# Performance work log

Hardware: AMD Instinct MI355X
Metric: run time of the kernel (lower is better)

Reference implementation:

```python
import jax, jax.numpy as jnp
import numpy as np

N, L, E = 2, 2048, 1024
H = 16
HD = E // H
FF = 4 * E
EPS = 1e-5


def _layer_norm(x, g, b):
    mu = jnp.mean(x, axis=-1, keepdims=True)
    var = jnp.mean((x - mu) ** 2, axis=-1, keepdims=True)
    return (x - mu) * jax.lax.rsqrt(var + EPS) * g + b


def setup_inputs() -> dict:
    key = jax.random.key(0)
    ks = jax.random.split(key, 9)
    s = 0.02
    return {
        "value": jax.random.normal(ks[0], (N, L, E), jnp.float32),
        "key": jax.random.normal(ks[1], (N, L, E), jnp.float32),
        "query": jax.random.normal(ks[2], (N, L, E), jnp.float32),
        "w_out": jax.random.normal(ks[3], (E, E), jnp.float32) * s,
        "b_out": jnp.zeros((E,), jnp.float32),
        "w1": jax.random.normal(ks[4], (E, FF), jnp.float32) * s,
        "b1": jnp.zeros((FF,), jnp.float32),
        "w2": jax.random.normal(ks[5], (FF, E), jnp.float32) * s,
        "b2": jnp.zeros((E,), jnp.float32),
        "g1": jnp.ones((E,), jnp.float32),
        "be1": jnp.zeros((E,), jnp.float32),
        "g2": jnp.ones((E,), jnp.float32),
        "be2": jnp.zeros((E,), jnp.float32),
    }


def reference(value, key, query, w_out, b_out, w1, b1, w2, b2, g1, be1, g2, be2):
    # NOTE: source module never applies its Q/K/V Linear layers (repo bug);
    # raw inputs are reshaped per-head and used directly.
    v = value.reshape(N, L, H, HD)
    k = key.reshape(N, L, H, HD)
    q = query.reshape(N, L, H, HD)
    # energy: [N, H, Lq, Lk]; scale is 1/sqrt(embed_size) per the source
    energy = jnp.einsum("nqhd,nkhd->nhqk", q, k)
    attn = jax.nn.softmax(energy / jnp.sqrt(jnp.float32(E)), axis=-1)
    out = jnp.einsum("nhql,nlhd->nqhd", attn, v).reshape(N, L, E)
    out = out @ w_out + b_out
    x = _layer_norm(out + query, g1, be1)
    ff = jax.nn.relu(x @ w1 + b1) @ w2 + b2
    return _layer_norm(ff + x, g2, be2)
```

## Files before the change

kernel.cpp:

```cpp
#include <hip/hip_runtime.h>
#include <hip/hip_bf16.h>

#define NB 2
#define LL 2048
#define EE 1024
#define HH 16
#define HDD 64
#define FFD 4096

typedef unsigned short ushort_t;
typedef __attribute__((ext_vector_type(8))) short short8;
typedef __attribute__((ext_vector_type(4))) float f32x4;

constexpr float LN_EPS = 1e-5f;
constexpr float QSCALE = 0.03125f * 1.44269504088896340736f;

__device__ inline ushort_t f2bf(float f) {
    union { __hip_bfloat16 b; ushort_t u; } v;
    v.b = __float2bfloat16(f);
    return v.u;
}
__device__ inline float bf2f(unsigned us) {
    union { unsigned u; float f; } v; v.u = us << 16; return v.f;
}
__device__ inline unsigned pk_hi16(float lo, float hi) {
    const unsigned sel = 0x07060302u;
    unsigned r;
    asm("v_perm_b32 %0, %1, %2, %3" : "=v"(r) : "v"(hi), "v"(lo), "s"(sel));
    return r;
}

__device__ inline void gload16(const void* g, void* lds) {
    __builtin_amdgcn_global_load_lds(
        (const __attribute__((address_space(1))) void*)g,
        (__attribute__((address_space(3))) void*)lds, 16, 0, 0);
}

__global__ __launch_bounds__(256) void k_cvt(
    const float* __restrict__ in, ushort_t* __restrict__ out)
{
    const int t = threadIdx.x;
    const int g = blockIdx.x * 32 + (t >> 3);
    const int n = g >> 15, h = (g >> 11) & 15, l2 = g & 2047;
    const int d0 = (t & 7) * 8;
    const float* src = in + ((size_t)(n * LL + l2) * HH + h) * HDD + d0;
    const float4 a = *(const float4*)src;
    const float4 b = *(const float4*)(src + 4);
    uint4 pk;
    pk.x = f2bf(a.x) | ((unsigned)f2bf(a.y) << 16);
    pk.y = f2bf(a.z) | ((unsigned)f2bf(a.w) << 16);
    pk.z = f2bf(b.x) | ((unsigned)f2bf(b.y) << 16);
    pk.w = f2bf(b.z) | ((unsigned)f2bf(b.w) << 16);
    *(uint4*)(out + (size_t)g * HDD + d0) = pk;
}

__global__ __launch_bounds__(256) void v_cvt_t(
    const float* __restrict__ in, ushort_t* __restrict__ out)
{
    __shared__ float T[64][68];
    const int lb = blockIdx.x, h = blockIdx.y, n = blockIdx.z;
    const int t = threadIdx.x;
    const int l0 = lb * 64;
    {
        const int r = t >> 2, c0 = (t & 3) * 16;
        const float* src = in + ((size_t)(n * LL + l0 + r) * HH + h) * HDD + c0;
#pragma unroll
        for (int i = 0; i < 4; ++i)
            *(float4*)&T[r][c0 + 4 * i] = *(const float4*)(src + 4 * i);
    }
    __syncthreads();
    {
        const int d = t >> 2, tq = t & 3;
        unsigned u[8];
#pragma unroll
        for (int k = 0; k < 8; ++k) {
            const int c0 = tq * 16 + 2 * k, c1 = c0 + 1;
            const int p0 = (((c0 >> 5) * 2 + ((c0 >> 2) & 1)) << 4) +
                           (((c0 >> 3) & 3) << 2) + (c0 & 3);
            const int p1 = (((c1 >> 5) * 2 + ((c1 >> 2) & 1)) << 4) +
                           (((c1 >> 3) & 3) << 2) + (c1 & 3);
            u[k] = f2bf(T[p0][d]) | ((unsigned)f2bf(T[p1][d]) << 16);
        }
        ushort_t* dst = out + ((size_t)(n * HH + h) * HDD + d) * LL + l0 + tq * 16;
        uint4 q0; q0.x = u[0]; q0.y = u[1]; q0.z = u[2]; q0.w = u[3];
        uint4 q1; q1.x = u[4]; q1.y = u[5]; q1.z = u[6]; q1.w = u[7];
        *(uint4*)(dst)     = q0;
        *(uint4*)(dst + 8) = q1;
    }
}

__global__ __launch_bounds__(256) void attn_mfma(
    const float* __restrict__ Qf,
    const ushort_t* __restrict__ Kh,
    const ushort_t* __restrict__ Vt,
    ushort_t* __restrict__ O)
{
    const int s = blockIdx.x;
    const int xcd = s & 7, seq = s >> 3;
    const int qb = seq & 31, tt = seq >> 5;
    const int h = ((tt & 1) << 3) | xcd;
    const int n = tt >> 1;

    const int t = threadIdx.x, w = t >> 6, l = t & 63;
    const int lr = l & 15, lg = l >> 4;

    __shared__ __align__(16) ushort_t Ks[2][64 * 64];
    __shared__ __align__(16) ushort_t Vs[2][64 * 64];

    const size_t hbase = ((size_t)n * HH + h) * LL * HDD;
    const size_t vbase = ((size_t)n * HH + h) * HDD * LL;
    const int q0 = qb * 64 + w * 16;

    short8 bq[2];
#pragma unroll
    for (int ks = 0; ks < 2; ++ks) {
        const float* qsrc = Qf + ((size_t)(n * LL + q0 + lr) * HH + h) * HDD
                               + ks * 32 + lg * 8;
        const float4 a = *(const float4*)qsrc;
        const float4 b = *(const float4*)(qsrc + 4);
        union { short8 s8; unsigned u[4]; } pk;
        pk.u[0] = f2bf(a.x * QSCALE) | ((unsigned)f2bf(a.y * QSCALE) << 16);
        pk.u[1] = f2bf(a.z * QSCALE) | ((unsigned)f2bf(a.w * QSCALE) << 16);
        pk.u[2] = f2bf(b.x * QSCALE) | ((unsigned)f2bf(b.y * QSCALE) << 16);
        pk.u[3] = f2bf(b.z * QSCALE) | ((unsigned)f2bf(b.w * QSCALE) << 16);
        bq[ks] = pk.s8;
    }

    union { short8 s8; ushort_t u[8]; } one_u;
#pragma unroll
    for (int i = 0; i < 8; ++i) one_u.u[i] = 0x3F80;
    const short8 ones = one_u.s8;

    f32x4 acco[4];
#pragma unroll
    for (int dn = 0; dn < 4; ++dn) {
        f32x4 z = {0.f, 0.f, 0.f, 0.f};
        acco[dn] = z;
    }
    f32x4 accp = {0.f, 0.f, 0.f, 0.f};

    const int id0 = w * 2;
#define STAGE(buf, kt)                                                         \
    {                                                                          \
        _Pragma("unroll")                                                      \
        for (int j = 0; j < 2; ++j) {                                          \
            const int id = (id0 + j) * 64 + l;                                 \
            const int r = id >> 3, c = id & 7;                                 \
            const int cs = c ^ (r & 7);                                        \
            gload16(Kh + hbase + (size_t)((kt) * 64 + r) * HDD + cs * 8,       \
                    (void*)(Ks[buf] + (id0 + j) * 512));                       \
            gload16(Vt + vbase + (size_t)r * LL + (kt) * 64 + cs * 8,          \
                    (void*)(Vs[buf] + (id0 + j) * 512));                       \
        }                                                                      \
    }

    constexpr int NT = LL / 64;
    STAGE(0, 0);
    STAGE(1, 1);
    asm volatile("s_waitcnt vmcnt(4)" ::: "memory");
    __builtin_amdgcn_sched_barrier(0);
    __builtin_amdgcn_s_barrier();

    const f32x4 z4 = {0.f, 0.f, 0.f, 0.f};

    for (int kt = 0; kt < NT; ++kt) {
        const int buf = kt & 1;

        f32x4 accs[4];
        __builtin_amdgcn_s_setprio(1);
        {
            short8 ak[4];
#pragma unroll
            for (int nk = 0; nk < 4; ++nk) {
                const int row = nk * 16 + lr;
                ak[nk] = *(const short8*)(
                    Ks[buf] + row * 64 + ((lg) ^ (row & 7)) * 8);
            }
#pragma unroll
            for (int nk = 0; nk < 4; ++nk)
                accs[nk] = __builtin_amdgcn_mfma_f32_16x16x32_bf16(
                    ak[nk], bq[0], z4, 0, 0, 0);
#pragma unroll
            for (int nk = 0; nk < 4; ++nk) {
                const int row = nk * 16 + lr;
                ak[nk] = *(const short8*)(
                    Ks[buf] + row * 64 + ((4 | lg) ^ (row & 7)) * 8);
            }
#pragma unroll
            for (int nk = 0; nk < 4; ++nk)
                accs[nk] = __builtin_amdgcn_mfma_f32_16x16x32_bf16(
                    ak[nk], bq[1], accs[nk], 0, 0, 0);
        }
        __builtin_amdgcn_s_setprio(0);

        float p[4][4];
#pragma unroll
        for (int nk = 0; nk < 4; ++nk)
#pragma unroll
            for (int r = 0; r < 4; ++r)
                p[nk][r] = __builtin_amdgcn_exp2f(accs[nk][r]);
        short8 pa[2];
#pragma unroll
        for (int ks = 0; ks < 2; ++ks) {
            union { short8 s8; unsigned u[4]; } pk;
            pk.u[0] = pk_hi16(p[2*ks][0],   p[2*ks][1]);
            pk.u[1] = pk_hi16(p[2*ks][2],   p[2*ks][3]);
            pk.u[2] = pk_hi16(p[2*ks+1][0], p[2*ks+1][1]);
            pk.u[3] = pk_hi16(p[2*ks+1][2], p[2*ks+1][3]);
            pa[ks] = pk.s8;
        }

        __builtin_amdgcn_s_setprio(1);
#pragma unroll
        for (int ks = 0; ks < 2; ++ks) {
            short8 bv[4];
#pragma unroll
            for (int dn = 0; dn < 4; ++dn) {
                const int row = dn * 16 + lr;
                bv[dn] = *(const short8*)(
                    Vs[buf] + row * 64 + (((ks << 2) | lg) ^ (row & 7)) * 8);
            }
            accp = __builtin_amdgcn_mfma_f32_16x16x32_bf16(pa[ks], ones, accp,
                                                           0, 0, 0);
#pragma unroll
            for (int dn = 0; dn < 4; ++dn)
                acco[dn] = __builtin_amdgcn_mfma_f32_16x16x32_bf16(
                    pa[ks], bv[dn], acco[dn], 0, 0, 0);
        }
        __builtin_amdgcn_s_setprio(0);

        __builtin_amdgcn_s_barrier();
        STAGE(buf, kt + 2);
        asm volatile("s_waitcnt vmcnt(4)" ::: "memory");
        __builtin_amdgcn_sched_barrier(0);
        __builtin_amdgcn_s_barrier();
    }

#pragma unroll
    for (int r = 0; r < 4; ++r) {
        const float invl = 1.f / accp[r];
        const int qq = q0 + lg * 4 + r;
        ushort_t* dst = O + (size_t)(n * LL + qq) * EE + h * HDD + lr;
#pragma unroll
        for (int dn = 0; dn < 4; ++dn)
            dst[dn * 16] = f2bf(acco[dn][r] * invl);
    }
#undef STAGE
}

__global__ __launch_bounds__(256) void tcvt(
    const float* __restrict__ in, ushort_t* __restrict__ out, int K, int N)
{
    __shared__ float T[32][36];
    const int n0 = blockIdx.x * 32, k0 = blockIdx.y * 32;
    const int r = threadIdx.x >> 3, c4 = (threadIdx.x & 7) * 4;
    const float4 v = *(const float4*)(in + (size_t)(k0 + r) * N + n0 + c4);
    T[r][c4] = v.x; T[r][c4 + 1] = v.y; T[r][c4 + 2] = v.z; T[r][c4 + 3] = v.w;
    __syncthreads();
    const unsigned a = f2bf(T[c4][r])     | ((unsigned)f2bf(T[c4 + 1][r]) << 16);
    const unsigned b = f2bf(T[c4 + 2][r]) | ((unsigned)f2bf(T[c4 + 3][r]) << 16);
    uint2 pk; pk.x = a; pk.y = b;
    *(uint2*)(out + (size_t)(n0 + r) * K + k0 + c4) = pk;
}

__global__ __launch_bounds__(512, 2) void gemm8p(
    const ushort_t* __restrict__ A, const ushort_t* __restrict__ Bt,
    const float* __restrict__ bias, ushort_t* __restrict__ C,
    int M, int N, int K)
{
    __shared__ __align__(16) ushort_t L[2][4][256 * 32];

    const int tid = threadIdx.x;
    const int w = tid >> 6, l = tid & 63;
    const int fr = l & 15, lg = l >> 4;
    const int wr = w >> 2, wc = w & 3;

    const int gx = gridDim.x;
    const int nwg = gx * gridDim.y;
    const int bid = blockIdx.y * gx + blockIdx.x;
    int tile = bid;
    if ((nwg & 7) == 0) tile = (bid & 7) * (nwg >> 3) + (bid >> 3);
    const int bx = tile % gx, by = tile / gx;
    const int brow = by * 256, bcol = bx * 256;

    const int NT = K >> 6;
    const int UMAX = NT << 2;

#define STAGE8(u)                                                              \
    if ((u) < UMAX) {                                                          \
        const int tt = (u) >> 2, slot = (u) & 3;                               \
        const int op = slot & 1, kh = slot >> 1;                               \
        const ushort_t* sp = op ? Bt : A;                                      \
        const int rb = op ? bcol : brow;                                       \
        ushort_t* db = (ushort_t*)L[tt & 1][slot];                             \
        _Pragma("unroll")                                                      \
        for (int j = 0; j < 2; ++j) {                                          \
            const int id = j * 512 + tid;                                      \
            const int row = id >> 2, c = id & 3;                               \
            const int cs = c ^ ((row >> 1) & 3);                               \
            gload16(sp + (size_t)(rb + row) * K + tt * 64 + kh * 32 + cs * 8,  \
                    (void*)(db + id * 8));                                     \
        }                                                                      \
    }

    f32x4 acc[8][4];
#pragma unroll
    for (int i = 0; i < 8; ++i)
#pragma unroll
        for (int g = 0; g < 4; ++g) { f32x4 zz = {0.f,0.f,0.f,0.f}; acc[i][g] = zz; }

#pragma unroll
    for (int u = 0; u < 6; ++u) STAGE8(u);
    asm volatile("s_waitcnt vmcnt(4)" ::: "memory");
    __builtin_amdgcn_sched_barrier(0);
    __builtin_amdgcn_s_barrier();

    const int iters = NT >> 1;
    for (int it = 0; it < iters; ++it) {
#pragma unroll
        for (int p = 0; p < 8; ++p) {
            STAGE8(it * 8 + p + 6);
            const int d  = p >> 2;
            const int mh = p & 1, kh = (p >> 1) & 1;
            short8 af[4], bfr[4];
#pragma unroll
            for (int f = 0; f < 4; ++f) {
                const int row = wr * 128 + (mh * 4 + f) * 16 + fr;
                const int ch = lg ^ ((row >> 1) & 3);
                af[f] = *(const short8*)(&L[d][kh * 2][row * 32 + ch * 8]);
            }
#pragma unroll
            for (int g = 0; g < 4; ++g) {
                const int row = wc * 64 + g * 16 + fr;
                const int ch = lg ^ ((row >> 1) & 3);
                bfr[g] = *(const short8*)(&L[d][kh * 2 + 1][row * 32 + ch * 8]);
            }
            __builtin_amdgcn_s_barrier();
            __builtin_amdgcn_s_setprio(1);
#pragma unroll
            for (int f = 0; f < 4; ++f)
#pragma unroll
                for (int g = 0; g < 4; ++g)
                    acc[mh * 4 + f][g] = __builtin_amdgcn_mfma_f32_16x16x32_bf16(
                        af[f], bfr[g], acc[mh * 4 + f][g], 0, 0, 0);
            __builtin_amdgcn_s_setprio(0);
            if (p == 3 || p == 7) {
                asm volatile("s_waitcnt vmcnt(4)" ::: "memory");
                __builtin_amdgcn_sched_barrier(0);
            }
            __builtin_amdgcn_s_barrier();
        }
    }

#pragma unroll
    for (int mi = 0; mi < 8; ++mi) {
#pragma unroll
        for (int g = 0; g < 4; ++g) {
            const int col = bcol + wc * 64 + g * 16 + fr;
            const float bv = bias[col];
#pragma unroll
            for (int r = 0; r < 4; ++r) {
                const int row = brow + wr * 128 + mi * 16 + lg * 4 + r;
                const float v = fmaxf(acc[mi][g][r] + bv, 0.f);
                C[(size_t)row * N + col] = f2bf(v);
            }
        }
    }
#undef STAGE8
}

#define SOFF(slot) ((slot) == 0 ? 0 : (slot) == 1 ? 8192 : (slot) == 2 ? 12288 : 20480)

template <int KSPLIT>
__global__ __launch_bounds__(512, 2) void gemm8p_n128(
    const ushort_t* __restrict__ A, const ushort_t* __restrict__ Bt,
    ushort_t* __restrict__ C, int M, int N, int K)
{
    __shared__ __align__(16) ushort_t L[2][24576];

    const int tid = threadIdx.x;
    const int w = tid >> 6, l = tid & 63;
    const int fr = l & 15, lg = l >> 4;
    const int wr = w >> 2, wc = w & 3;

    const int z = blockIdx.z;
    const int Keff = K / KSPLIT;
    const int kb = z * Keff;

    const int gx = gridDim.x;
    const int nwg = gx * gridDim.y;
    const int bid = blockIdx.y * gx + blockIdx.x;
    int tile = bid;
    if ((nwg & 7) == 0) tile = (bid & 7) * (nwg >> 3) + (bid >> 3);
    const int bx = tile % gx, by = tile / gx;
    const int brow = by * 256, bcol = bx * 128;

    const int NT = Keff >> 6;
    const int UMAX = NT << 2;

#define STG(u)                                                                 \
    if ((u) < UMAX) {                                                          \
        const int tt = (u) >> 2, slot = (u) & 3;                               \
        const int op = slot & 1, kh = slot >> 1;                               \
        const ushort_t* sp = op ? Bt : A;                                      \
        const int rb = op ? bcol : brow;                                       \
        ushort_t* db = (ushort_t*)L[tt & 1] + SOFF(slot);                      \
        const int nld = op ? 1 : 2;                                            \
        _Pragma("unroll")                                                      \
        for (int j = 0; j < nld; ++j) {                                        \
            const int id = j * 512 + tid;                                      \
            const int row = id >> 2, c = id & 3;                               \
            const int cs = c ^ ((row >> 1) & 3);                               \
            gload16(sp + (size_t)(rb + row) * K + kb + tt * 64 + kh * 32 + cs * 8, \
                    (void*)(db + id * 8));                                     \
        }                                                                      \
    }

    f32x4 acc[8][2];
#pragma unroll
    for (int i = 0; i < 8; ++i)
#pragma unroll
        for (int g = 0; g < 2; ++g) { f32x4 zz = {0.f,0.f,0.f,0.f}; acc[i][g] = zz; }

#pragma unroll
    for (int u = 0; u < 6; ++u) STG(u);
    asm volatile("s_waitcnt vmcnt(3)" ::: "memory");
    __builtin_amdgcn_sched_barrier(0);
    __builtin_amdgcn_s_barrier();

    const int iters = NT >> 1;
    for (int it = 0; it < iters; ++it) {
#pragma unroll
        for (int p = 0; p < 8; ++p) {
            STG(it * 8 + p + 6);
            const int d  = p >> 2;
            const int mh = p & 1, kh = (p >> 1) & 1;
            short8 af[4], bfr[2];
#pragma unroll
            for (int f = 0; f < 4; ++f) {
                const int row = wr * 128 + (mh * 4 + f) * 16 + fr;
                const int ch = lg ^ ((row >> 1) & 3);
                af[f] = *(const short8*)(&L[d][SOFF(kh * 2) + row * 32 + ch * 8]);
            }
#pragma unroll
            for (int g = 0; g < 2; ++g) {
                const int row = wc * 32 + g * 16 + fr;
                const int ch = lg ^ ((row >> 1) & 3);
                bfr[g] = *(const short8*)(&L[d][SOFF(kh * 2 + 1) + row * 32 + ch * 8]);
            }
            __builtin_amdgcn_s_barrier();
            __builtin_amdgcn_s_setprio(1);
#pragma unroll
            for (int f = 0; f < 4; ++f)
#pragma unroll
                for (int g = 0; g < 2; ++g)
                    acc[mh * 4 + f][g] = __builtin_amdgcn_mfma_f32_16x16x32_bf16(
                        af[f], bfr[g], acc[mh * 4 + f][g], 0, 0, 0);
            __builtin_amdgcn_s_setprio(0);
            if (p == 3 || p == 7) {
                asm volatile("s_waitcnt vmcnt(3)" ::: "memory");
                __builtin_amdgcn_sched_barrier(0);
            }
            __builtin_amdgcn_s_barrier();
        }
    }

    ushort_t* Cb = C + (size_t)z * M * N;
#pragma unroll
    for (int mi = 0; mi < 8; ++mi) {
#pragma unroll
        for (int g = 0; g < 2; ++g) {
            const int col = bcol + wc * 32 + g * 16 + fr;
#pragma unroll
            for (int r = 0; r < 4; ++r) {
                const int row = brow + wr * 128 + mi * 16 + lg * 4 + r;
                Cb[(size_t)row * N + col] = f2bf(acc[mi][g][r]);
            }
        }
    }
#undef STG
}

__global__ __launch_bounds__(256) void ln_mid(
    const ushort_t* __restrict__ y0, const ushort_t* __restrict__ y1,
    const float* __restrict__ qres, const float* __restrict__ b0,
    const float* __restrict__ g, const float* __restrict__ b,
    ushort_t* __restrict__ out)
{
    const int row = blockIdx.x;
    const int t = threadIdx.x;
    const size_t off = (size_t)row * EE;
    const uint2 a = ((const uint2*)(y0 + off))[t];
    const uint2 c = ((const uint2*)(y1 + off))[t];
    const float4 qq = ((const float4*)(qres + off))[t];
    const float4 b04 = ((const float4*)b0)[t];
    float x[4];
    x[0] = bf2f(a.x & 0xffff) + bf2f(c.x & 0xffff) + qq.x + b04.x;
    x[1] = bf2f(a.x >> 16)    + bf2f(c.x >> 16)    + qq.y + b04.y;
    x[2] = bf2f(a.y & 0xffff) + bf2f(c.y & 0xffff) + qq.z + b04.z;
    x[3] = bf2f(a.y >> 16)    + bf2f(c.y >> 16)    + qq.w + b04.w;

    float s = 0.f, ss = 0.f;
#pragma unroll
    for (int i = 0; i < 4; ++i) { s += x[i]; ss += x[i] * x[i]; }
#pragma unroll
    for (int o = 1; o < 64; o <<= 1) {
        s  += __shfl_xor(s, o, 64);
        ss += __shfl_xor(ss, o, 64);
    }
    __shared__ float sm[8];
    const int wid = t >> 6;
    if ((t & 63) == 0) { sm[wid * 2] = s; sm[wid * 2 + 1] = ss; }
    __syncthreads();
    const float stot  = sm[0] + sm[2] + sm[4] + sm[6];
    const float sstot = sm[1] + sm[3] + sm[5] + sm[7];
    const float mu  = stot * (1.f / EE);
    const float inv = rsqrtf(sstot * (1.f / EE) - mu * mu + LN_EPS);

    const float4 gg = ((const float4*)g)[t];
    const float4 bb = ((const float4*)b)[t];
    uint2 pk;
    pk.x = f2bf((x[0] - mu) * inv * gg.x + bb.x) |
           ((unsigned)f2bf((x[1] - mu) * inv * gg.y + bb.y) << 16);
    pk.y = f2bf((x[2] - mu) * inv * gg.z + bb.z) |
           ((unsigned)f2bf((x[3] - mu) * inv * gg.w + bb.w) << 16);
    ((uint2*)(out + off))[t] = pk;
}

__global__ __launch_bounds__(256) void ln_out(
    const ushort_t* __restrict__ y0, const ushort_t* __restrict__ y1,
    const ushort_t* __restrict__ xb, const float* __restrict__ b2,
    const float* __restrict__ g, const float* __restrict__ be,
    float* __restrict__ out)
{
    const int row = blockIdx.x;
    const int t = threadIdx.x;
    const size_t off = (size_t)row * EE;
    const uint2 a = ((const uint2*)(y0 + off))[t];
    const uint2 b = ((const uint2*)(y1 + off))[t];
    const uint2 c = ((const uint2*)(xb + off))[t];
    const float4 bb2 = ((const float4*)b2)[t];
    float x[4];
    x[0] = bf2f(a.x & 0xffff) + bf2f(b.x & 0xffff) + bf2f(c.x & 0xffff) + bb2.x;
    x[1] = bf2f(a.x >> 16)    + bf2f(b.x >> 16)    + bf2f(c.x >> 16)    + bb2.y;
    x[2] = bf2f(a.y & 0xffff) + bf2f(b.y & 0xffff) + bf2f(c.y & 0xffff) + bb2.z;
    x[3] = bf2f(a.y >> 16)    + bf2f(b.y >> 16)    + bf2f(c.y >> 16)    + bb2.w;

    float s = 0.f, ss = 0.f;
#pragma unroll
    for (int i = 0; i < 4; ++i) { s += x[i]; ss += x[i] * x[i]; }
#pragma unroll
    for (int o = 1; o < 64; o <<= 1) {
        s  += __shfl_xor(s, o, 64);
        ss += __shfl_xor(ss, o, 64);
    }
    __shared__ float sm[8];
    const int wid = t >> 6;
    if ((t & 63) == 0) { sm[wid * 2] = s; sm[wid * 2 + 1] = ss; }
    __syncthreads();
    const float stot  = sm[0] + sm[2] + sm[4] + sm[6];
    const float sstot = sm[1] + sm[3] + sm[5] + sm[7];
    const float mu  = stot * (1.f / EE);
    const float inv = rsqrtf(sstot * (1.f / EE) - mu * mu + LN_EPS);

    const float4 gg = ((const float4*)g)[t];
    const float4 bb = ((const float4*)be)[t];
    float4 o;
    o.x = (x[0] - mu) * inv * gg.x + bb.x;
    o.y = (x[1] - mu) * inv * gg.y + bb.y;
    o.z = (x[2] - mu) * inv * gg.z + bb.z;
    o.w = (x[3] - mu) * inv * gg.w + bb.w;
    ((float4*)(out + off))[t] = o;
}

extern "C" void kernel_launch(void* const* d_in, const int* in_sizes, int n_in,
                              void* d_out, int out_size, void* d_ws, size_t ws_size,
                              hipStream_t stream) {
    (void)in_sizes; (void)n_in; (void)out_size; (void)ws_size;
    const float* value = (const float*)d_in[0];
    const float* key   = (const float*)d_in[1];
    const float* query = (const float*)d_in[2];
    const float* w_out = (const float*)d_in[3];
    const float* b_out = (const float*)d_in[4];
    const float* w1    = (const float*)d_in[5];
    const float* b1    = (const float*)d_in[6];
    const float* w2    = (const float*)d_in[7];
    const float* b2    = (const float*)d_in[8];
    const float* g1    = (const float*)d_in[9];
    const float* be1   = (const float*)d_in[10];
    const float* g2    = (const float*)d_in[11];
    const float* be2   = (const float*)d_in[12];
    float* out = (float*)d_out;

    const int M = NB * LL;
    char* base = (char*)d_ws;
    ushort_t* attn_bf = (ushort_t*)(base);
    ushort_t* x_bf    = (ushort_t*)(base + (8ull  << 20));
    char*     hregion = base + (16ull << 20);
    ushort_t* h_bf    = (ushort_t*)hregion;
    ushort_t* Kh      = (ushort_t*)(hregion);
    ushort_t* Vt      = (ushort_t*)(hregion + (8ull  << 20));
    ushort_t* y01     = (ushort_t*)(base + (48ull << 20));
    ushort_t* w0T     = (ushort_t*)(base + (64ull << 20));
    ushort_t* w1T     = (ushort_t*)(base + (66ull << 20));
    ushort_t* w2T     = (ushort_t*)(base + (74ull << 20));

    tcvt<<<dim3(EE / 32, EE / 32), 256, 0, stream>>>(w_out, w0T, EE, EE);
    tcvt<<<dim3(FFD / 32, EE / 32), 256, 0, stream>>>(w1, w1T, EE, FFD);
    tcvt<<<dim3(EE / 32, FFD / 32), 256, 0, stream>>>(w2, w2T, FFD, EE);

    k_cvt<<<NB * HH * LL / 32, 256, 0, stream>>>(key, Kh);
    v_cvt_t<<<dim3(LL / 64, HH, NB), 256, 0, stream>>>(value, Vt);

    attn_mfma<<<dim3(NB * HH * LL / 64), 256, 0, stream>>>(query, Kh, Vt,
                                                           attn_bf);

    gemm8p_n128<2><<<dim3(EE / 128, M / 256, 2), 512, 0, stream>>>(
        attn_bf, w0T, y01, M, EE, EE);
    ln_mid<<<M, 256, 0, stream>>>(y01, y01 + (size_t)M * EE, query, b_out,
                                  g1, be1, x_bf);

    gemm8p<<<dim3(FFD / 256, M / 256), 512, 0, stream>>>(x_bf, w1T, b1, h_bf,
                                                         M, FFD, EE);
    gemm8p_n128<2><<<dim3(EE / 128, M / 256, 2), 512, 0, stream>>>(
        h_bf, w2T, y01, M, EE, FFD);
    ln_out<<<M, 256, 0, stream>>>(y01, y01 + (size_t)M * EE, x_bf, b2, g2, be2,
                                  out);
}
```

Baseline: 189.7 us.

## Process two query sub-tiles per warp in attention to reuse K/V fragments

Each warp in the attention kernel now handles 32 query rows (two 16-row sub-tiles) instead of 16, so each block covers 128 queries and the grid is halved. K and V fragments loaded from shared memory are reused across both sub-tiles, which halves LDS reads and global K/V staging per unit of work. In exchange, register pressure roughly doubles for the accumulators and only 512 blocks are launched, which lowers occupancy and parallelism across CUs.

```diff
diff --git a/kernel.cpp b/kernel.cpp
--- a/kernel.cpp
+++ b/kernel.cpp
@@ -97,7 +97,7 @@
 {
     const int s = blockIdx.x;
     const int xcd = s & 7, seq = s >> 3;
-    const int qb = seq & 31, tt = seq >> 5;
+    const int qb = seq & 15, tt = seq >> 4;
     const int h = ((tt & 1) << 3) | xcd;
     const int n = tt >> 1;
 
@@ -109,35 +109,42 @@
 
     const size_t hbase = ((size_t)n * HH + h) * LL * HDD;
     const size_t vbase = ((size_t)n * HH + h) * HDD * LL;
-    const int q0 = qb * 64 + w * 16;
-
-    short8 bq[2];
-#pragma unroll
-    for (int ks = 0; ks < 2; ++ks) {
-        const float* qsrc = Qf + ((size_t)(n * LL + q0 + lr) * HH + h) * HDD
-                               + ks * 32 + lg * 8;
-        const float4 a = *(const float4*)qsrc;
-        const float4 b = *(const float4*)(qsrc + 4);
-        union { short8 s8; unsigned u[4]; } pk;
-        pk.u[0] = f2bf(a.x * QSCALE) | ((unsigned)f2bf(a.y * QSCALE) << 16);
-        pk.u[1] = f2bf(a.z * QSCALE) | ((unsigned)f2bf(a.w * QSCALE) << 16);
-        pk.u[2] = f2bf(b.x * QSCALE) | ((unsigned)f2bf(b.y * QSCALE) << 16);
-        pk.u[3] = f2bf(b.z * QSCALE) | ((unsigned)f2bf(b.w * QSCALE) << 16);
-        bq[ks] = pk.s8;
-    }
+    const int q0 = qb * 128 + w * 32;
+
+    short8 bq[2][2];
+#pragma unroll
+    for (int mi = 0; mi < 2; ++mi)
+#pragma unroll
+        for (int ks = 0; ks < 2; ++ks) {
+            const float* qsrc = Qf +
+                ((size_t)(n * LL + q0 + mi * 16 + lr) * HH + h) * HDD
+                + ks * 32 + lg * 8;
+            const float4 a = *(const float4*)qsrc;
+            const float4 b = *(const float4*)(qsrc + 4);
+            union { short8 s8; unsigned u[4]; } pk;
+            pk.u[0] = f2bf(a.x * QSCALE) | ((unsigned)f2bf(a.y * QSCALE) << 16);
+            pk.u[1] = f2bf(a.z * QSCALE) | ((unsigned)f2bf(a.w * QSCALE) << 16);
+            pk.u[2] = f2bf(b.x * QSCALE) | ((unsigned)f2bf(b.y * QSCALE) << 16);
+            pk.u[3] = f2bf(b.z * QSCALE) | ((unsigned)f2bf(b.w * QSCALE) << 16);
+            bq[mi][ks] = pk.s8;
+        }
 
     union { short8 s8; ushort_t u[8]; } one_u;
 #pragma unroll
     for (int i = 0; i < 8; ++i) one_u.u[i] = 0x3F80;
     const short8 ones = one_u.s8;
 
-    f32x4 acco[4];
-#pragma unroll
-    for (int dn = 0; dn < 4; ++dn) {
-        f32x4 z = {0.f, 0.f, 0.f, 0.f};
-        acco[dn] = z;
-    }
-    f32x4 accp = {0.f, 0.f, 0.f, 0.f};
+    f32x4 acco[2][4];
+#pragma unroll
+    for (int mi = 0; mi < 2; ++mi)
+#pragma unroll
+        for (int dn = 0; dn < 4; ++dn) {
+            f32x4 z = {0.f, 0.f, 0.f, 0.f};
+            acco[mi][dn] = z;
+        }
+    f32x4 accp[2];
+    accp[0] = (f32x4){0.f, 0.f, 0.f, 0.f};
+    accp[1] = (f32x4){0.f, 0.f, 0.f, 0.f};
 
     const int id0 = w * 2;
 #define STAGE(buf, kt)                                                         \
@@ -166,7 +173,7 @@
     for (int kt = 0; kt < NT; ++kt) {
         const int buf = kt & 1;
 
-        f32x4 accs[4];
+        f32x4 accs[2][4];
         __builtin_amdgcn_s_setprio(1);
         {
             short8 ak[4];
@@ -177,9 +184,12 @@
                     Ks[buf] + row * 64 + ((lg) ^ (row & 7)) * 8);
             }
 #pragma unroll
-            for (int nk = 0; nk < 4; ++nk)
-                accs[nk] = __builtin_amdgcn_mfma_f32_16x16x32_bf16(
-                    ak[nk], bq[0], z4, 0, 0, 0);
+            for (int nk = 0; nk < 4; ++nk) {
+                accs[0][nk] = __builtin_amdgcn_mfma_f32_16x16x32_bf16(
+                    ak[nk], bq[0][0], z4, 0, 0, 0);
+                accs[1][nk] = __builtin_amdgcn_mfma_f32_16x16x32_bf16(
+                    ak[nk], bq[1][0], z4, 0, 0, 0);
+            }
 #pragma unroll
             for (int nk = 0; nk < 4; ++nk) {
                 const int row = nk * 16 + lr;
@@ -187,27 +197,33 @@
                     Ks[buf] + row * 64 + ((4 | lg) ^ (row & 7)) * 8);
             }
 #pragma unroll
+            for (int nk = 0; nk < 4; ++nk) {
+                accs[0][nk] = __builtin_amdgcn_mfma_f32_16x16x32_bf16(
+                    ak[nk], bq[0][1], accs[0][nk], 0, 0, 0);
+                accs[1][nk] = __builtin_amdgcn_mfma_f32_16x16x32_bf16(
+                    ak[nk], bq[1][1], accs[1][nk], 0, 0, 0);
+            }
+        }
+        __builtin_amdgcn_s_setprio(0);
+
+        short8 pa[2][2];
+#pragma unroll
+        for (int mi = 0; mi < 2; ++mi) {
+            float p[4][4];
+#pragma unroll
             for (int nk = 0; nk < 4; ++nk)
-                accs[nk] = __builtin_amdgcn_mfma_f32_16x16x32_bf16(
-                    ak[nk], bq[1], accs[nk], 0, 0, 0);
-        }
-        __builtin_amdgcn_s_setprio(0);
-
-        float p[4][4];
-#pragma unroll
-        for (int nk = 0; nk < 4; ++nk)
-#pragma unroll
-            for (int r = 0; r < 4; ++r)
-                p[nk][r] = __builtin_amdgcn_exp2f(accs[nk][r]);
-        short8 pa[2];
-#pragma unroll
-        for (int ks = 0; ks < 2; ++ks) {
-            union { short8 s8; unsigned u[4]; } pk;
-            pk.u[0] = pk_hi16(p[2*ks][0],   p[2*ks][1]);
-            pk.u[1] = pk_hi16(p[2*ks][2],   p[2*ks][3]);
-            pk.u[2] = pk_hi16(p[2*ks+1][0], p[2*ks+1][1]);
-            pk.u[3] = pk_hi16(p[2*ks+1][2], p[2*ks+1][3]);
-            pa[ks] = pk.s8;
+#pragma unroll
+                for (int r = 0; r < 4; ++r)
+                    p[nk][r] = __builtin_amdgcn_exp2f(accs[mi][nk][r]);
+#pragma unroll
+            for (int ks = 0; ks < 2; ++ks) {
+                union { short8 s8; unsigned u[4]; } pk;
+                pk.u[0] = pk_hi16(p[2*ks][0],   p[2*ks][1]);
+                pk.u[1] = pk_hi16(p[2*ks][2],   p[2*ks][3]);
+                pk.u[2] = pk_hi16(p[2*ks+1][0], p[2*ks+1][1]);
+                pk.u[3] = pk_hi16(p[2*ks+1][2], p[2*ks+1][3]);
+                pa[mi][ks] = pk.s8;
+            }
         }
 
         __builtin_amdgcn_s_setprio(1);
@@ -220,12 +236,17 @@
                 bv[dn] = *(const short8*)(
                     Vs[buf] + row * 64 + (((ks << 2) | lg) ^ (row & 7)) * 8);
             }
-            accp = __builtin_amdgcn_mfma_f32_16x16x32_bf16(pa[ks], ones, accp,
-                                                           0, 0, 0);
-#pragma unroll
-            for (int dn = 0; dn < 4; ++dn)
-                acco[dn] = __builtin_amdgcn_mfma_f32_16x16x32_bf16(
-                    pa[ks], bv[dn], acco[dn], 0, 0, 0);
+            accp[0] = __builtin_amdgcn_mfma_f32_16x16x32_bf16(
+                pa[0][ks], ones, accp[0], 0, 0, 0);
+            accp[1] = __builtin_amdgcn_mfma_f32_16x16x32_bf16(
+                pa[1][ks], ones, accp[1], 0, 0, 0);
+#pragma unroll
+            for (int dn = 0; dn < 4; ++dn) {
+                acco[0][dn] = __builtin_amdgcn_mfma_f32_16x16x32_bf16(
+                    pa[0][ks], bv[dn], acco[0][dn], 0, 0, 0);
+                acco[1][dn] = __builtin_amdgcn_mfma_f32_16x16x32_bf16(
+                    pa[1][ks], bv[dn], acco[1][dn], 0, 0, 0);
+            }
         }
         __builtin_amdgcn_s_setprio(0);
 
@@ -237,13 +258,16 @@
     }
 
 #pragma unroll
-    for (int r = 0; r < 4; ++r) {
-        const float invl = 1.f / accp[r];
-        const int qq = q0 + lg * 4 + r;
-        ushort_t* dst = O + (size_t)(n * LL + qq) * EE + h * HDD + lr;
-#pragma unroll
-        for (int dn = 0; dn < 4; ++dn)
-            dst[dn * 16] = f2bf(acco[dn][r] * invl);
+    for (int mi = 0; mi < 2; ++mi) {
+#pragma unroll
+        for (int r = 0; r < 4; ++r) {
+            const float invl = 1.f / accp[mi][r];
+            const int qq = q0 + mi * 16 + lg * 4 + r;
+            ushort_t* dst = O + (size_t)(n * LL + qq) * EE + h * HDD + lr;
+#pragma unroll
+            for (int dn = 0; dn < 4; ++dn)
+                dst[dn * 16] = f2bf(acco[mi][dn][r] * invl);
+        }
     }
 #undef STAGE
 }
@@ -612,8 +636,8 @@
     k_cvt<<<NB * HH * LL / 32, 256, 0, stream>>>(key, Kh);
     v_cvt_t<<<dim3(LL / 64, HH, NB), 256, 0, stream>>>(value, Vt);
 
-    attn_mfma<<<dim3(NB * HH * LL / 64), 256, 0, stream>>>(query, Kh, Vt,
-                                                           attn_bf);
+    attn_mfma<<<dim3(NB * HH * LL / 128), 256, 0, stream>>>(query, Kh, Vt,
+                                                            attn_bf);
 
     gemm8p_n128<2><<<dim3(EE / 128, M / 256, 2), 512, 0, stream>>>(
         attn_bf, w0T, y01, M, EE, EE);
```

Result: faster. 186.0 us (-2.0%).

## Software-pipeline QK^T one tile ahead of PV with triple-buffered K

Applied to the files above, without the earlier changes.

Restructures the attention main loop so the QK^T MFMAs for the next key tile are issued before the exp/PV work of the current tile. K gets a third LDS buffer and V keeps two, and the loop is manually unrolled by two to ping-pong the score accumulators. The goal is to overlap the matrix-core work with the exp2 and pack ALU work and hide LDS latency. The cost is more LDS, more live registers, and a more complex K/V prefetch schedule. The prefetch also runs past the end of the sequence, as the original loop already did.

```diff
diff --git a/kernel.cpp b/kernel.cpp
--- a/kernel.cpp
+++ b/kernel.cpp
@@ -104,8 +104,8 @@
     const int t = threadIdx.x, w = t >> 6, l = t & 63;
     const int lr = l & 15, lg = l >> 4;
 
-    __shared__ __align__(16) ushort_t Ks[2][64 * 64];
-    __shared__ __align__(16) ushort_t Vs[2][64 * 64];
+    __shared__ __align__(16) ushort_t Kl[3][64 * 64];
+    __shared__ __align__(16) ushort_t Vl[2][64 * 64];
 
     const size_t hbase = ((size_t)n * HH + h) * LL * HDD;
     const size_t vbase = ((size_t)n * HH + h) * HDD * LL;
@@ -140,7 +140,7 @@
     f32x4 accp = {0.f, 0.f, 0.f, 0.f};
 
     const int id0 = w * 2;
-#define STAGE(buf, kt)                                                         \
+#define STAGEK(buf, kt)                                                        \
     {                                                                          \
         _Pragma("unroll")                                                      \
         for (int j = 0; j < 2; ++j) {                                          \
@@ -148,92 +148,131 @@
             const int r = id >> 3, c = id & 7;                                 \
             const int cs = c ^ (r & 7);                                        \
             gload16(Kh + hbase + (size_t)((kt) * 64 + r) * HDD + cs * 8,       \
-                    (void*)(Ks[buf] + (id0 + j) * 512));                       \
+                    (void*)(Kl[buf] + (id0 + j) * 512));                       \
+        }                                                                      \
+    }
+#define STAGEV(buf, kt)                                                        \
+    {                                                                          \
+        _Pragma("unroll")                                                      \
+        for (int j = 0; j < 2; ++j) {                                          \
+            const int id = (id0 + j) * 64 + l;                                 \
+            const int r = id >> 3, c = id & 7;                                 \
+            const int cs = c ^ (r & 7);                                        \
             gload16(Vt + vbase + (size_t)r * LL + (kt) * 64 + cs * 8,          \
-                    (void*)(Vs[buf] + (id0 + j) * 512));                       \
+                    (void*)(Vl[buf] + (id0 + j) * 512));                       \
         }                                                                      \
     }
 
     constexpr int NT = LL / 64;
-    STAGE(0, 0);
-    STAGE(1, 1);
+    const f32x4 z4 = {0.f, 0.f, 0.f, 0.f};
+
+    STAGEK(0, 0);
+    STAGEK(1, 1);
+    STAGEV(0, 0);
+    STAGEK(2, 2);
+    STAGEV(1, 1);
     asm volatile("s_waitcnt vmcnt(4)" ::: "memory");
     __builtin_amdgcn_sched_barrier(0);
     __builtin_amdgcn_s_barrier();
 
-    const f32x4 z4 = {0.f, 0.f, 0.f, 0.f};
-
-    for (int kt = 0; kt < NT; ++kt) {
-        const int buf = kt & 1;
-
-        f32x4 accs[4];
-        __builtin_amdgcn_s_setprio(1);
-        {
-            short8 ak[4];
-#pragma unroll
-            for (int nk = 0; nk < 4; ++nk) {
-                const int row = nk * 16 + lr;
-                ak[nk] = *(const short8*)(
-                    Ks[buf] + row * 64 + ((lg) ^ (row & 7)) * 8);
-            }
-#pragma unroll
-            for (int nk = 0; nk < 4; ++nk)
-                accs[nk] = __builtin_amdgcn_mfma_f32_16x16x32_bf16(
-                    ak[nk], bq[0], z4, 0, 0, 0);
-#pragma unroll
-            for (int nk = 0; nk < 4; ++nk) {
-                const int row = nk * 16 + lr;
-                ak[nk] = *(const short8*)(
-                    Ks[buf] + row * 64 + ((4 | lg) ^ (row & 7)) * 8);
-            }
-#pragma unroll
-            for (int nk = 0; nk < 4; ++nk)
-                accs[nk] = __builtin_amdgcn_mfma_f32_16x16x32_bf16(
-                    ak[nk], bq[1], accs[nk], 0, 0, 0);
+    f32x4 accsA[4], accsB[4];
+    {
+        short8 ak[4];
+#pragma unroll
+        for (int nk = 0; nk < 4; ++nk) {
+            const int row = nk * 16 + lr;
+            ak[nk] = *(const short8*)(Kl[0] + row * 64 + ((lg) ^ (row & 7)) * 8);
         }
-        __builtin_amdgcn_s_setprio(0);
-
-        float p[4][4];
 #pragma unroll
         for (int nk = 0; nk < 4; ++nk)
-#pragma unroll
-            for (int r = 0; r < 4; ++r)
-                p[nk][r] = __builtin_amdgcn_exp2f(accs[nk][r]);
-        short8 pa[2];
-#pragma unroll
-        for (int ks = 0; ks < 2; ++ks) {
-            union { short8 s8; unsigned u[4]; } pk;
-            pk.u[0] = pk_hi16(p[2*ks][0],   p[2*ks][1]);
-            pk.u[1] = pk_hi16(p[2*ks][2],   p[2*ks][3]);
-            pk.u[2] = pk_hi16(p[2*ks+1][0], p[2*ks+1][1]);
-            pk.u[3] = pk_hi16(p[2*ks+1][2], p[2*ks+1][3]);
-            pa[ks] = pk.s8;
+            accsA[nk] = __builtin_amdgcn_mfma_f32_16x16x32_bf16(
+                ak[nk], bq[0], z4, 0, 0, 0);
+#pragma unroll
+        for (int nk = 0; nk < 4; ++nk) {
+            const int row = nk * 16 + lr;
+            ak[nk] = *(const short8*)(Kl[0] + row * 64 + ((4 | lg) ^ (row & 7)) * 8);
         }
-
-        __builtin_amdgcn_s_setprio(1);
-#pragma unroll
-        for (int ks = 0; ks < 2; ++ks) {
-            short8 bv[4];
-#pragma unroll
-            for (int dn = 0; dn < 4; ++dn) {
-                const int row = dn * 16 + lr;
-                bv[dn] = *(const short8*)(
-                    Vs[buf] + row * 64 + (((ks << 2) | lg) ^ (row & 7)) * 8);
-            }
-            accp = __builtin_amdgcn_mfma_f32_16x16x32_bf16(pa[ks], ones, accp,
-                                                           0, 0, 0);
-#pragma unroll
-            for (int dn = 0; dn < 4; ++dn)
-                acco[dn] = __builtin_amdgcn_mfma_f32_16x16x32_bf16(
-                    pa[ks], bv[dn], acco[dn], 0, 0, 0);
-        }
-        __builtin_amdgcn_s_setprio(0);
-
-        __builtin_amdgcn_s_barrier();
-        STAGE(buf, kt + 2);
-        asm volatile("s_waitcnt vmcnt(4)" ::: "memory");
-        __builtin_amdgcn_sched_barrier(0);
-        __builtin_amdgcn_s_barrier();
+#pragma unroll
+        for (int nk = 0; nk < 4; ++nk)
+            accsA[nk] = __builtin_amdgcn_mfma_f32_16x16x32_bf16(
+                ak[nk], bq[1], accsA[nk], 0, 0, 0);
+    }
+
+    int ks3 = 0, kn = 1;
+
+#define ATTN_BODY(O_, N_, VB_, KT_)                                            \
+    {                                                                          \
+        const ushort_t* kb_ = Kl[kn];                                          \
+        __builtin_amdgcn_s_setprio(1);                                         \
+        {                                                                      \
+            short8 ak[4];                                                      \
+            _Pragma("unroll")                                                  \
+            for (int nk = 0; nk < 4; ++nk) {                                   \
+                const int row = nk * 16 + lr;                                  \
+                ak[nk] = *(const short8*)(kb_ + row * 64 + ((lg) ^ (row & 7)) * 8); \
+            }                                                                  \
+            _Pragma("unroll")                                                  \
+            for (int nk = 0; nk < 4; ++nk)                                     \
+                N_[nk] = __builtin_amdgcn_mfma_f32_16x16x32_bf16(              \
+                    ak[nk], bq[0], z4, 0, 0, 0);                               \
+            _Pragma("unroll")                                                  \
+            for (int nk = 0; nk < 4; ++nk) {                                   \
+                const int row = nk * 16 + lr;                                  \
+                ak[nk] = *(const short8*)(kb_ + row * 64 + ((4 | lg) ^ (row & 7)) * 8); \
+            }                                                                  \
+            _Pragma("unroll")                                                  \
+            for (int nk = 0; nk < 4; ++nk)                                     \
+                N_[nk] = __builtin_amdgcn_mfma_f32_16x16x32_bf16(              \
+                    ak[nk], bq[1], N_[nk], 0, 0, 0);                           \
+        }                                                                      \
+        __builtin_amdgcn_s_setprio(0);                                         \
+        float p[4][4];                                                         \
+        _Pragma("unroll")                                                      \
+        for (int nk = 0; nk < 4; ++nk) {                                       \
+            _Pragma("unroll")                                                  \
+            for (int r = 0; r < 4; ++r)                                        \
+                p[nk][r] = __builtin_amdgcn_exp2f(O_[nk][r]);                  \
+        }                                                                      \
+        short8 pa[2];                                                          \
+        _Pragma("unroll")                                                      \
+        for (int ks2 = 0; ks2 < 2; ++ks2) {                                    \
+            union { short8 s8; unsigned u[4]; } pk;                            \
+            pk.u[0] = pk_hi16(p[2 * ks2][0], p[2 * ks2][1]);                   \
+            pk.u[1] = pk_hi16(p[2 * ks2][2], p[2 * ks2][3]);                   \
+            pk.u[2] = pk_hi16(p[2 * ks2 + 1][0], p[2 * ks2 + 1][1]);           \
+            pk.u[3] = pk_hi16(p[2 * ks2 + 1][2], p[2 * ks2 + 1][3]);           \
+            pa[ks2] = pk.s8;                                                   \
+        }                                                                      \
+        __builtin_amdgcn_s_setprio(1);                                         \
+        _Pragma("unroll")                                                      \
+        for (int ks2 = 0; ks2 < 2; ++ks2) {                                    \
+            short8 bv[4];                                                      \
+            _Pragma("unroll")                                                  \
+            for (int dn = 0; dn < 4; ++dn) {                                   \
+                const int row = dn * 16 + lr;                                  \
+                bv[dn] = *(const short8*)(                                     \
+                    Vl[VB_] + row * 64 + (((ks2 << 2) | lg) ^ (row & 7)) * 8); \
+            }                                                                  \
+            accp = __builtin_amdgcn_mfma_f32_16x16x32_bf16(pa[ks2], ones,      \
+                                                           accp, 0, 0, 0);    \
+            _Pragma("unroll")                                                  \
+            for (int dn = 0; dn < 4; ++dn)                                     \
+                acco[dn] = __builtin_amdgcn_mfma_f32_16x16x32_bf16(            \
+                    pa[ks2], bv[dn], acco[dn], 0, 0, 0);                       \
+        }                                                                      \
+        __builtin_amdgcn_s_setprio(0);                                         \
+        __builtin_amdgcn_s_barrier();                                          \
+        STAGEK(ks3, (KT_) + 3);                                                \
+        STAGEV(VB_, (KT_) + 2);                                                \
+        asm volatile("s_waitcnt vmcnt(4)" ::: "memory");                       \
+        __builtin_amdgcn_sched_barrier(0);                                     \
+        __builtin_amdgcn_s_barrier();                                          \
+        { const int tnk = kn + 1; ks3 = kn; kn = (tnk == 3) ? 0 : tnk; }       \
+    }
+
+    for (int kt = 0; kt < NT; kt += 2) {
+        ATTN_BODY(accsA, accsB, 0, kt);
+        ATTN_BODY(accsB, accsA, 1, kt + 1);
     }
 
 #pragma unroll
@@ -245,7 +284,9 @@
         for (int dn = 0; dn < 4; ++dn)
             dst[dn * 16] = f2bf(acco[dn][r] * invl);
     }
-#undef STAGE
+#undef ATTN_BODY
+#undef STAGEK
+#undef STAGEV
 }
 
 __global__ __launch_bounds__(256) void tcvt(
```

After: 187.1 us. About the same (-1.4%).
